# Performance work log

Hardware: AMD Instinct MI355X
Metric: run time of the kernel (lower is better)

## Reference

```python
import jax, jax.numpy as jnp
import numpy as np

N_NODES = 50000
N_EDGES = 600000
D_FEAT = 128


def setup_inputs() -> dict:
    key = jax.random.key(0)
    ks = jax.random.split(key, 10)
    x = jax.random.normal(ks[0], (N_NODES, D_FEAT), dtype=jnp.float32)
    src = jax.random.randint(ks[1], (N_EDGES,), 0, N_NODES, dtype=jnp.int32)
    dst = jax.random.randint(ks[2], (N_EDGES,), 0, N_NODES, dtype=jnp.int32)
    w1 = jax.random.normal(ks[3], (1, D_FEAT), dtype=jnp.float32) * 0.05
    Wd1 = jax.random.normal(ks[4], (D_FEAT, 64), dtype=jnp.float32) * 0.05
    b1 = jnp.zeros((64,), dtype=jnp.float32)
    w2 = jax.random.normal(ks[5], (1, 64), dtype=jnp.float32) * 0.05
    Wd2 = jax.random.normal(ks[6], (64, 32), dtype=jnp.float32) * 0.05
    b2 = jnp.zeros((32,), dtype=jnp.float32)
    Wout = jax.random.normal(ks[7], (32, 4), dtype=jnp.float32) * 0.05
    bout = jnp.zeros((4,), dtype=jnp.float32)
    return {"x": x, "src": src, "dst": dst, "w1": w1, "Wd1": Wd1, "b1": b1,
            "w2": w2, "Wd2": Wd2, "b2": b2, "Wout": Wout, "bout": bout}


def _spmm(src, dst, h):
    # A @ h for COO adjacency (edge src -> dst contributes h[src] into row dst)
    return jax.ops.segment_sum(h[src], dst, num_segments=N_NODES)


def reference(x, src, dst, w1, Wd1, b1, w2, Wd2, b2, Wout, bout):
    # input_layer is an Input wrapper: identity. Dropout is identity at inference.
    h = _spmm(src, dst, x) * w1          # GraphLayer 1: SpMM + elementwise scale
    h = h @ Wd1 + b1                     # Dense(64), linear activation
    h = _spmm(src, dst, h) * w2          # GraphLayer 2
    h = h @ Wd2 + b2                     # Dense(32)
    logits = h @ Wout + bout             # Dense(4)
    return jax.nn.softmax(logits, axis=-1)
```

## Files before the change

### kernel.cpp

```cpp
#include <hip/hip_runtime.h>
#include <hip/hip_bf16.h>

#define D_FEAT 128
#define NP 64
#define NP_SHIFT 6
#define P_PARTS 782
#define CAP 1024
#define EPB 2048


__global__ __launch_bounds__(256) void fused_xw_bucket_kernel(
    const float4* __restrict__ x4,
    const int* __restrict__ src,
    const int* __restrict__ dst,
    const float* __restrict__ w1,  const float* __restrict__ Wd1,
    const float* __restrict__ b1,  const float* __restrict__ w2,
    const float* __restrict__ Wd2, const float* __restrict__ b2,
    const float* __restrict__ Wout, const float* __restrict__ bout,
    int* __restrict__ partFill, int* __restrict__ edgeBuf,
    float* __restrict__ gc, float4* __restrict__ u4,
    int nN, int nE, int xwBlocks)
{
    __shared__ int sm[2 * P_PARTS];
    int t = threadIdx.x;

    if ((int)blockIdx.x < xwBlocks) {
        float* T2   = (float*)sm;
        float* Wall = (float*)sm + 256;
        {
            int m = t >> 2, j = t & 3;
            float s = 0.f;
            for (int p = 0; p < 32; ++p) s += Wd2[m * 32 + p] * Wout[p * 4 + j];
            T2[t] = w2[m] * s;
        }
        __syncthreads();
        for (int idx = t; idx < 512; idx += 256) {
            int k = idx >> 2, j = idx & 3;
            float s = 0.f;
            for (int m = 0; m < 64; ++m) s += Wd1[k * 64 + m] * T2[m * 4 + j];
            Wall[idx] = w1[k] * s;
        }
        if (blockIdx.x == 0 && t < 4) {
            float s = 0.f;
            for (int m = 0; m < 64; ++m) s += b1[m] * T2[m * 4 + t];
            gc[t] = s;
            float s2 = 0.f;
            for (int p = 0; p < 32; ++p) s2 += b2[p] * Wout[p * 4 + t];
            gc[4 + t] = s2 + bout[t];
        }
        __syncthreads();
        int r = blockIdx.x * 256 + t;
        if (r < nN) {
            const float4* W = (const float4*)Wall;
            float4 acc = make_float4(0.f, 0.f, 0.f, 0.f);
            #pragma unroll 8
            for (int k4 = 0; k4 < 32; ++k4) {
                float4 xv = x4[(size_t)r * 32 + k4];
                float4 w0 = W[4 * k4 + 0];
                float4 wv1 = W[4 * k4 + 1];
                float4 wv2 = W[4 * k4 + 2];
                float4 wv3 = W[4 * k4 + 3];
                acc.x += xv.x * w0.x + xv.y * wv1.x + xv.z * wv2.x + xv.w * wv3.x;
                acc.y += xv.x * w0.y + xv.y * wv1.y + xv.z * wv2.y + xv.w * wv3.y;
                acc.z += xv.x * w0.z + xv.y * wv1.z + xv.z * wv2.z + xv.w * wv3.z;
                acc.w += xv.x * w0.w + xv.y * wv1.w + xv.z * wv2.w + xv.w * wv3.w;
            }
            u4[r] = acc;
        }
    } else {
        int b = blockIdx.x - xwBlocks;
        int* hist = sm;
        int* base = sm + P_PARTS;
        for (int p = t; p < P_PARTS; p += 256) hist[p] = 0;
        __syncthreads();
        int beg = b * EPB + t;
        int end = min(b * EPB + EPB, nE);
        for (int i = beg; i < end; i += 256)
            atomicAdd(&hist[dst[i] >> NP_SHIFT], 1);
        __syncthreads();
        for (int p = t; p < P_PARTS; p += 256) {
            int h = hist[p];
            base[p] = h ? atomicAdd(&partFill[p], h) : 0;
        }
        __syncthreads();
        for (int i = beg; i < end; i += 256) {
            int d = dst[i];
            int p = d >> NP_SHIFT;
            int rank = atomicSub(&hist[p], 1) - 1;
            int pos = base[p] + rank;
            if (pos < CAP)
                edgeBuf[p * CAP + pos] = src[i] | ((d & (NP - 1)) << 16);
        }
    }
}

__global__ __launch_bounds__(256) void spmm_part_kernel(
    const int* __restrict__ partFill,
    const int* __restrict__ edgeBuf,
    const float4* __restrict__ in4,
    const float* __restrict__ gc, int gcOff,
    float4* __restrict__ out4, int nN, int doSoftmax)
{
    __shared__ float acc[NP * 4];
    int t = threadIdx.x, p = blockIdx.x;
    acc[t] = 0.f;
    __syncthreads();
    int n = min(partFill[p], CAP);
    const int* eb = edgeBuf + p * CAP;
    for (int i = t; i < n; i += 256) {
        int e = eb[i];
        float4 val = in4[e & 0xFFFF];
        int dl = e >> 16;
        atomicAdd(&acc[dl * 4 + 0], val.x);
        atomicAdd(&acc[dl * 4 + 1], val.y);
        atomicAdd(&acc[dl * 4 + 2], val.z);
        atomicAdd(&acc[dl * 4 + 3], val.w);
    }
    __syncthreads();
    if (t < NP) {
        int node = p * NP + t;
        if (node < nN) {
            float4 a = ((const float4*)acc)[t];
            float lx = a.x + gc[gcOff + 0];
            float ly = a.y + gc[gcOff + 1];
            float lz = a.z + gc[gcOff + 2];
            float lw = a.w + gc[gcOff + 3];
            if (doSoftmax) {
                float m = fmaxf(fmaxf(lx, ly), fmaxf(lz, lw));
                float ex = __expf(lx - m);
                float ey = __expf(ly - m);
                float ez = __expf(lz - m);
                float ew = __expf(lw - m);
                float r = 1.f / (ex + ey + ez + ew);
                out4[node] = make_float4(ex * r, ey * r, ez * r, ew * r);
            } else {
                out4[node] = make_float4(lx, ly, lz, lw);
            }
        }
    }
}

extern "C" void kernel_launch(void* const* d_in, const int* in_sizes, int n_in,
                              void* d_out, int out_size, void* d_ws, size_t ws_size,
                              hipStream_t stream)
{
    const float* x    = (const float*)d_in[0];
    const int*   src  = (const int*)d_in[1];
    const int*   dst  = (const int*)d_in[2];
    const float* w1   = (const float*)d_in[3];
    const float* Wd1  = (const float*)d_in[4];
    const float* b1   = (const float*)d_in[5];
    const float* w2   = (const float*)d_in[6];
    const float* Wd2  = (const float*)d_in[7];
    const float* b2   = (const float*)d_in[8];
    const float* Wout = (const float*)d_in[9];
    const float* bout = (const float*)d_in[10];

    const int nE = in_sizes[1];
    const int nN = in_sizes[0] / D_FEAT;

    float* ws = (float*)d_ws;
    float* gc = ws;
    float* u  = ws + 16;
    float* v  = u + (size_t)nN * 4;
    int* partFill = (int*)(v + (size_t)nN * 4);
    int* edgeBuf  = partFill + ((P_PARTS + 63) & ~63);

    const int xwBlocks = (nN + 255) / 256;
    const int bkBlocks = (nE + EPB - 1) / EPB;

    hipMemsetAsync(partFill, 0, P_PARTS * sizeof(int), stream);
    fused_xw_bucket_kernel<<<xwBlocks + bkBlocks, 256, 0, stream>>>(
        (const float4*)x, src, dst, w1, Wd1, b1, w2, Wd2, b2, Wout, bout,
        partFill, edgeBuf, gc, (float4*)u, nN, nE, xwBlocks);
    spmm_part_kernel<<<P_PARTS, 256, 0, stream>>>(partFill, edgeBuf,
                                                  (const float4*)u, gc, 0,
                                                  (float4*)v, nN, 0);
    spmm_part_kernel<<<P_PARTS, 256, 0, stream>>>(partFill, edgeBuf,
                                                  (const float4*)v, gc, 4,
                                                  (float4*)d_out, nN, 1);
}
```

Before: 143.9 us.

## Replace partition bucketing with direct global-atomic edge scatter and separate softmax

Drops the dst-partition bucketing pass and the per-partition shared-memory SpMM, and instead scatters each edge directly into the node outputs with global float atomics, processing two edges per thread. The dense projection now gives each node row to 32 lanes with coalesced loads and a shuffle reduction, and it pre-initialises the outputs with the folded bias constants so the atomics can accumulate on top. The softmax moves into its own small kernel. This removes the bucketing and the CAP truncation, which silently dropped edges when a partition held more than 1024, but it trades them for many contended global atomics on random addresses and one extra launch.

```diff
diff --git a/kernel.cpp b/kernel.cpp
--- a/kernel.cpp
+++ b/kernel.cpp
@@ -1,142 +1,124 @@
 #include <hip/hip_runtime.h>
-#include <hip/hip_bf16.h>
 
 #define D_FEAT 128
-#define NP 64
-#define NP_SHIFT 6
-#define P_PARTS 782
-#define CAP 1024
-#define EPB 2048
 
 
-__global__ __launch_bounds__(256) void fused_xw_bucket_kernel(
+__global__ __launch_bounds__(256) void fold_xw_init_kernel(
     const float4* __restrict__ x4,
-    const int* __restrict__ src,
-    const int* __restrict__ dst,
     const float* __restrict__ w1,  const float* __restrict__ Wd1,
     const float* __restrict__ b1,  const float* __restrict__ w2,
     const float* __restrict__ Wd2, const float* __restrict__ b2,
     const float* __restrict__ Wout, const float* __restrict__ bout,
-    int* __restrict__ partFill, int* __restrict__ edgeBuf,
-    float* __restrict__ gc, float4* __restrict__ u4,
-    int nN, int nE, int xwBlocks)
+    float4* __restrict__ u4, float4* __restrict__ v4, float4* __restrict__ l4,
+    int nN)
 {
-    __shared__ int sm[2 * P_PARTS];
+    __shared__ float  T2[256];
+    __shared__ float4 W4[128];
+    __shared__ float4 gcs[2];
     int t = threadIdx.x;
 
-    if ((int)blockIdx.x < xwBlocks) {
-        float* T2   = (float*)sm;
-        float* Wall = (float*)sm + 256;
-        {
-            int m = t >> 2, j = t & 3;
-            float s = 0.f;
-            for (int p = 0; p < 32; ++p) s += Wd2[m * 32 + p] * Wout[p * 4 + j];
-            T2[t] = w2[m] * s;
+    {
+        int m = t >> 2, j = t & 3;
+        float s = 0.f;
+        for (int p = 0; p < 32; ++p) s += Wd2[m * 32 + p] * Wout[p * 4 + j];
+        T2[t] = w2[m] * s;
+    }
+    __syncthreads();
+    for (int idx = t; idx < 512; idx += 256) {
+        int k = idx >> 2, j = idx & 3;
+        float s = 0.f;
+        for (int m = 0; m < 64; ++m) s += Wd1[k * 64 + m] * T2[m * 4 + j];
+        ((float*)W4)[idx] = w1[k] * s;
+    }
+    if (t < 4) {
+        float s = 0.f;
+        for (int m = 0; m < 64; ++m) s += b1[m] * T2[m * 4 + t];
+        ((float*)gcs)[t] = s;
+        float s2 = 0.f;
+        for (int p = 0; p < 32; ++p) s2 += b2[p] * Wout[p * 4 + t];
+        ((float*)gcs)[4 + t] = s2 + bout[t];
+    }
+    __syncthreads();
+
+    int lane = t & 63;
+    int k4 = lane & 31;
+    float4 wa = W4[4 * k4 + 0];
+    float4 wb = W4[4 * k4 + 1];
+    float4 wc = W4[4 * k4 + 2];
+    float4 wd = W4[4 * k4 + 3];
+    float4 gv = gcs[0], cv = gcs[1];
+
+    int R0 = blockIdx.x * 256;
+    #pragma unroll 4
+    for (int p = 0; p < 32; ++p) {
+        int fi = R0 * 32 + p * 256 + t;
+        int r  = R0 + p * 8 + (t >> 5);
+        bool ok = r < nN;
+        float4 xv = ok ? x4[fi] : make_float4(0.f, 0.f, 0.f, 0.f);
+        float4 a;
+        a.x = xv.x * wa.x + xv.y * wb.x + xv.z * wc.x + xv.w * wd.x;
+        a.y = xv.x * wa.y + xv.y * wb.y + xv.z * wc.y + xv.w * wd.y;
+        a.z = xv.x * wa.z + xv.y * wb.z + xv.z * wc.z + xv.w * wd.z;
+        a.w = xv.x * wa.w + xv.y * wb.w + xv.z * wc.w + xv.w * wd.w;
+        for (int m = 16; m >= 1; m >>= 1) {
+            a.x += __shfl_xor(a.x, m);
+            a.y += __shfl_xor(a.y, m);
+            a.z += __shfl_xor(a.z, m);
+            a.w += __shfl_xor(a.w, m);
         }
-        __syncthreads();
-        for (int idx = t; idx < 512; idx += 256) {
-            int k = idx >> 2, j = idx & 3;
-            float s = 0.f;
-            for (int m = 0; m < 64; ++m) s += Wd1[k * 64 + m] * T2[m * 4 + j];
-            Wall[idx] = w1[k] * s;
-        }
-        if (blockIdx.x == 0 && t < 4) {
-            float s = 0.f;
-            for (int m = 0; m < 64; ++m) s += b1[m] * T2[m * 4 + t];
-            gc[t] = s;
-            float s2 = 0.f;
-            for (int p = 0; p < 32; ++p) s2 += b2[p] * Wout[p * 4 + t];
-            gc[4 + t] = s2 + bout[t];
-        }
-        __syncthreads();
-        int r = blockIdx.x * 256 + t;
-        if (r < nN) {
-            const float4* W = (const float4*)Wall;
-            float4 acc = make_float4(0.f, 0.f, 0.f, 0.f);
-            #pragma unroll 8
-            for (int k4 = 0; k4 < 32; ++k4) {
-                float4 xv = x4[(size_t)r * 32 + k4];
-                float4 w0 = W[4 * k4 + 0];
-                float4 wv1 = W[4 * k4 + 1];
-                float4 wv2 = W[4 * k4 + 2];
-                float4 wv3 = W[4 * k4 + 3];
-                acc.x += xv.x * w0.x + xv.y * wv1.x + xv.z * wv2.x + xv.w * wv3.x;
-                acc.y += xv.x * w0.y + xv.y * wv1.y + xv.z * wv2.y + xv.w * wv3.y;
-                acc.z += xv.x * w0.z + xv.y * wv1.z + xv.z * wv2.z + xv.w * wv3.z;
-                acc.w += xv.x * w0.w + xv.y * wv1.w + xv.z * wv2.w + xv.w * wv3.w;
-            }
-            u4[r] = acc;
-        }
-    } else {
-        int b = blockIdx.x - xwBlocks;
-        int* hist = sm;
-        int* base = sm + P_PARTS;
-        for (int p = t; p < P_PARTS; p += 256) hist[p] = 0;
-        __syncthreads();
-        int beg = b * EPB + t;
-        int end = min(b * EPB + EPB, nE);
-        for (int i = beg; i < end; i += 256)
-            atomicAdd(&hist[dst[i] >> NP_SHIFT], 1);
-        __syncthreads();
-        for (int p = t; p < P_PARTS; p += 256) {
-            int h = hist[p];
-            base[p] = h ? atomicAdd(&partFill[p], h) : 0;
-        }
-        __syncthreads();
-        for (int i = beg; i < end; i += 256) {
-            int d = dst[i];
-            int p = d >> NP_SHIFT;
-            int rank = atomicSub(&hist[p], 1) - 1;
-            int pos = base[p] + rank;
-            if (pos < CAP)
-                edgeBuf[p * CAP + pos] = src[i] | ((d & (NP - 1)) << 16);
+        if (ok && (lane & 31) == 0) {
+            u4[r] = a;
+            v4[r] = gv;
+            l4[r] = cv;
         }
     }
 }
 
-__global__ __launch_bounds__(256) void spmm_part_kernel(
-    const int* __restrict__ partFill,
-    const int* __restrict__ edgeBuf,
-    const float4* __restrict__ in4,
-    const float* __restrict__ gc, int gcOff,
-    float4* __restrict__ out4, int nN, int doSoftmax)
+__global__ __launch_bounds__(256) void edge_kernel(
+    const int2* __restrict__ src2, const int2* __restrict__ dst2,
+    const float4* __restrict__ in4, float* __restrict__ outp,
+    int nPair, int nE)
 {
-    __shared__ float acc[NP * 4];
-    int t = threadIdx.x, p = blockIdx.x;
-    acc[t] = 0.f;
-    __syncthreads();
-    int n = min(partFill[p], CAP);
-    const int* eb = edgeBuf + p * CAP;
-    for (int i = t; i < n; i += 256) {
-        int e = eb[i];
-        float4 val = in4[e & 0xFFFF];
-        int dl = e >> 16;
-        atomicAdd(&acc[dl * 4 + 0], val.x);
-        atomicAdd(&acc[dl * 4 + 1], val.y);
-        atomicAdd(&acc[dl * 4 + 2], val.z);
-        atomicAdd(&acc[dl * 4 + 3], val.w);
+    int i = blockIdx.x * 256 + threadIdx.x;
+    if (i < nPair) {
+        int2 s = src2[i];
+        int2 d = dst2[i];
+        float4 a = in4[s.x];
+        float4 b = in4[s.y];
+        atomicAdd(&outp[4 * d.x + 0], a.x);
+        atomicAdd(&outp[4 * d.x + 1], a.y);
+        atomicAdd(&outp[4 * d.x + 2], a.z);
+        atomicAdd(&outp[4 * d.x + 3], a.w);
+        atomicAdd(&outp[4 * d.y + 0], b.x);
+        atomicAdd(&outp[4 * d.y + 1], b.y);
+        atomicAdd(&outp[4 * d.y + 2], b.z);
+        atomicAdd(&outp[4 * d.y + 3], b.w);
     }
-    __syncthreads();
-    if (t < NP) {
-        int node = p * NP + t;
-        if (node < nN) {
-            float4 a = ((const float4*)acc)[t];
-            float lx = a.x + gc[gcOff + 0];
-            float ly = a.y + gc[gcOff + 1];
-            float lz = a.z + gc[gcOff + 2];
-            float lw = a.w + gc[gcOff + 3];
-            if (doSoftmax) {
-                float m = fmaxf(fmaxf(lx, ly), fmaxf(lz, lw));
-                float ex = __expf(lx - m);
-                float ey = __expf(ly - m);
-                float ez = __expf(lz - m);
-                float ew = __expf(lw - m);
-                float r = 1.f / (ex + ey + ez + ew);
-                out4[node] = make_float4(ex * r, ey * r, ez * r, ew * r);
-            } else {
-                out4[node] = make_float4(lx, ly, lz, lw);
-            }
-        }
+    if (i == 0 && (nE & 1)) {
+        int e = nE - 1;
+        int s = ((const int*)src2)[e];
+        int d = ((const int*)dst2)[e];
+        float4 a = in4[s];
+        atomicAdd(&outp[4 * d + 0], a.x);
+        atomicAdd(&outp[4 * d + 1], a.y);
+        atomicAdd(&outp[4 * d + 2], a.z);
+        atomicAdd(&outp[4 * d + 3], a.w);
+    }
+}
+
+__global__ __launch_bounds__(256) void softmax_kernel(
+    const float4* __restrict__ l4, float4* __restrict__ out4, int nN)
+{
+    int i = blockIdx.x * 256 + threadIdx.x;
+    if (i < nN) {
+        float4 l = l4[i];
+        float m  = fmaxf(fmaxf(l.x, l.y), fmaxf(l.z, l.w));
+        float ex = __expf(l.x - m);
+        float ey = __expf(l.y - m);
+        float ez = __expf(l.z - m);
+        float ew = __expf(l.w - m);
+        float r  = 1.f / (ex + ey + ez + ew);
+        out4[i] = make_float4(ex * r, ey * r, ez * r, ew * r);
     }
 }
 
@@ -160,23 +142,21 @@
     const int nN = in_sizes[0] / D_FEAT;
 
     float* ws = (float*)d_ws;
-    float* gc = ws;
-    float* u  = ws + 16;
+    float* u  = ws;
     float* v  = u + (size_t)nN * 4;
-    int* partFill = (int*)(v + (size_t)nN * 4);
-    int* edgeBuf  = partFill + ((P_PARTS + 63) & ~63);
+    float* l  = v + (size_t)nN * 4;
 
-    const int xwBlocks = (nN + 255) / 256;
-    const int bkBlocks = (nE + EPB - 1) / EPB;
+    const int nodeBlocks = (nN + 255) / 256;
+    const int nPair      = nE >> 1;
+    const int edgeBlocks = (nPair + 255) / 256;
 
-    hipMemsetAsync(partFill, 0, P_PARTS * sizeof(int), stream);
-    fused_xw_bucket_kernel<<<xwBlocks + bkBlocks, 256, 0, stream>>>(
-        (const float4*)x, src, dst, w1, Wd1, b1, w2, Wd2, b2, Wout, bout,
-        partFill, edgeBuf, gc, (float4*)u, nN, nE, xwBlocks);
-    spmm_part_kernel<<<P_PARTS, 256, 0, stream>>>(partFill, edgeBuf,
-                                                  (const float4*)u, gc, 0,
-                                                  (float4*)v, nN, 0);
-    spmm_part_kernel<<<P_PARTS, 256, 0, stream>>>(partFill, edgeBuf,
-                                                  (const float4*)v, gc, 4,
-                                                  (float4*)d_out, nN, 1);
+    fold_xw_init_kernel<<<nodeBlocks, 256, 0, stream>>>(
+        (const float4*)x, w1, Wd1, b1, w2, Wd2, b2, Wout, bout,
+        (float4*)u, (float4*)v, (float4*)l, nN);
+    edge_kernel<<<edgeBlocks, 256, 0, stream>>>(
+        (const int2*)src, (const int2*)dst, (const float4*)u, v, nPair, nE);
+    edge_kernel<<<edgeBlocks, 256, 0, stream>>>(
+        (const int2*)src, (const int2*)dst, (const float4*)v, l, nPair, nE);
+    softmax_kernel<<<nodeBlocks, 256, 0, stream>>>(
+        (const float4*)l, (float4*)d_out, nN);
 }
```

Result: slower. 361.0 us (+150.9%).

## Vectorize edge loads, pad partition counters, and transpose shared accumulators

Applied to the files above, without the earlier changes.

The bucketing phase now loads eight dst and src indices per thread with int4 vector loads held in registers. Previously each edge was read from global memory twice, once for the histogram and once for the scatter. Global partition fill counters are padded to 64-byte stride, which is meant to cut contention between atomics on the same cache line. The SpMM shared accumulator is transposed to [4][72], which is meant to reduce LDS bank conflicts on the atomic adds. The trade-offs are a larger memset and workspace offset and somewhat higher register use.

```diff
diff --git a/kernel.cpp b/kernel.cpp
--- a/kernel.cpp
+++ b/kernel.cpp
@@ -1,5 +1,4 @@
 #include <hip/hip_runtime.h>
-#include <hip/hip_bf16.h>
 
 #define D_FEAT 128
 #define NP 64
@@ -7,6 +6,7 @@
 #define P_PARTS 782
 #define CAP 1024
 #define EPB 2048
+#define PF_STRIDE 16
 
 
 __global__ __launch_bounds__(256) void fused_xw_bucket_kernel(
@@ -21,7 +21,7 @@
     float* __restrict__ gc, float4* __restrict__ u4,
     int nN, int nE, int xwBlocks)
 {
-    __shared__ int sm[2 * P_PARTS];
+    __shared__ __align__(16) int sm[2 * P_PARTS];
     int t = threadIdx.x;
 
     if ((int)blockIdx.x < xwBlocks) {
@@ -56,7 +56,7 @@
             #pragma unroll 8
             for (int k4 = 0; k4 < 32; ++k4) {
                 float4 xv = x4[(size_t)r * 32 + k4];
-                float4 w0 = W[4 * k4 + 0];
+                float4 w0  = W[4 * k4 + 0];
                 float4 wv1 = W[4 * k4 + 1];
                 float4 wv2 = W[4 * k4 + 2];
                 float4 wv3 = W[4 * k4 + 3];
@@ -73,23 +73,42 @@
         int* base = sm + P_PARTS;
         for (int p = t; p < P_PARTS; p += 256) hist[p] = 0;
         __syncthreads();
-        int beg = b * EPB + t;
-        int end = min(b * EPB + EPB, nE);
-        for (int i = beg; i < end; i += 256)
-            atomicAdd(&hist[dst[i] >> NP_SHIFT], 1);
+
+        int beg = b * EPB;
+        int i0  = beg + 8 * t;
+        int4 d0 = make_int4(0,0,0,0), d1 = make_int4(0,0,0,0);
+        int4 s0 = make_int4(0,0,0,0), s1 = make_int4(0,0,0,0);
+        if (i0 + 3 < nE) { d0 = ((const int4*)dst)[(beg >> 2) + 2 * t];
+                           s0 = ((const int4*)src)[(beg >> 2) + 2 * t]; }
+        else for (int j = 0; i0 + j < nE && j < 4; ++j) {
+            ((int*)&d0)[j] = dst[i0 + j]; ((int*)&s0)[j] = src[i0 + j];
+        }
+        if (i0 + 7 < nE) { d1 = ((const int4*)dst)[(beg >> 2) + 2 * t + 1];
+                           s1 = ((const int4*)src)[(beg >> 2) + 2 * t + 1]; }
+        else for (int j = 4; i0 + j < nE && j < 8; ++j) {
+            ((int*)&d1)[j - 4] = dst[i0 + j]; ((int*)&s1)[j - 4] = src[i0 + j];
+        }
+        int dd[8] = {d0.x, d0.y, d0.z, d0.w, d1.x, d1.y, d1.z, d1.w};
+        int ss[8] = {s0.x, s0.y, s0.z, s0.w, s1.x, s1.y, s1.z, s1.w};
+
+        #pragma unroll
+        for (int j = 0; j < 8; ++j)
+            if (i0 + j < nE) atomicAdd(&hist[dd[j] >> NP_SHIFT], 1);
         __syncthreads();
         for (int p = t; p < P_PARTS; p += 256) {
             int h = hist[p];
-            base[p] = h ? atomicAdd(&partFill[p], h) : 0;
-        }
-        __syncthreads();
-        for (int i = beg; i < end; i += 256) {
-            int d = dst[i];
-            int p = d >> NP_SHIFT;
-            int rank = atomicSub(&hist[p], 1) - 1;
-            int pos = base[p] + rank;
-            if (pos < CAP)
-                edgeBuf[p * CAP + pos] = src[i] | ((d & (NP - 1)) << 16);
+            base[p] = h ? atomicAdd(&partFill[p * PF_STRIDE], h) : 0;
+        }
+        __syncthreads();
+        #pragma unroll
+        for (int j = 0; j < 8; ++j) {
+            if (i0 + j < nE) {
+                int d = dd[j], pp = d >> NP_SHIFT;
+                int rank = atomicSub(&hist[pp], 1) - 1;
+                int pos = base[pp] + rank;
+                if (pos < CAP)
+                    edgeBuf[pp * CAP + pos] = ss[j] | ((d & (NP - 1)) << 16);
+            }
         }
     }
 }
@@ -101,30 +120,29 @@
     const float* __restrict__ gc, int gcOff,
     float4* __restrict__ out4, int nN, int doSoftmax)
 {
-    __shared__ float acc[NP * 4];
+    __shared__ float acc[4][72];
     int t = threadIdx.x, p = blockIdx.x;
-    acc[t] = 0.f;
+    for (int i = t; i < 288; i += 256) ((float*)acc)[i] = 0.f;
     __syncthreads();
-    int n = min(partFill[p], CAP);
+    int n = min(partFill[p * PF_STRIDE], CAP);
     const int* eb = edgeBuf + p * CAP;
     for (int i = t; i < n; i += 256) {
         int e = eb[i];
         float4 val = in4[e & 0xFFFF];
         int dl = e >> 16;
-        atomicAdd(&acc[dl * 4 + 0], val.x);
-        atomicAdd(&acc[dl * 4 + 1], val.y);
-        atomicAdd(&acc[dl * 4 + 2], val.z);
-        atomicAdd(&acc[dl * 4 + 3], val.w);
+        atomicAdd(&acc[0][dl], val.x);
+        atomicAdd(&acc[1][dl], val.y);
+        atomicAdd(&acc[2][dl], val.z);
+        atomicAdd(&acc[3][dl], val.w);
     }
     __syncthreads();
     if (t < NP) {
         int node = p * NP + t;
         if (node < nN) {
-            float4 a = ((const float4*)acc)[t];
-            float lx = a.x + gc[gcOff + 0];
-            float ly = a.y + gc[gcOff + 1];
-            float lz = a.z + gc[gcOff + 2];
-            float lw = a.w + gc[gcOff + 3];
+            float lx = acc[0][t] + gc[gcOff + 0];
+            float ly = acc[1][t] + gc[gcOff + 1];
+            float lz = acc[2][t] + gc[gcOff + 2];
+            float lw = acc[3][t] + gc[gcOff + 3];
             if (doSoftmax) {
                 float m = fmaxf(fmaxf(lx, ly), fmaxf(lz, lw));
                 float ex = __expf(lx - m);
@@ -164,12 +182,12 @@
     float* u  = ws + 16;
     float* v  = u + (size_t)nN * 4;
     int* partFill = (int*)(v + (size_t)nN * 4);
-    int* edgeBuf  = partFill + ((P_PARTS + 63) & ~63);
+    int* edgeBuf  = partFill + P_PARTS * PF_STRIDE;
 
     const int xwBlocks = (nN + 255) / 256;
     const int bkBlocks = (nE + EPB - 1) / EPB;
 
-    hipMemsetAsync(partFill, 0, P_PARTS * sizeof(int), stream);
+    hipMemsetAsync(partFill, 0, P_PARTS * PF_STRIDE * sizeof(int), stream);
     fused_xw_bucket_kernel<<<xwBlocks + bkBlocks, 256, 0, stream>>>(
         (const float4*)x, src, dst, w1, Wd1, b1, w2, Wd2, b2, Wout, bout,
         partFill, edgeBuf, gc, (float4*)u, nN, nE, xwBlocks);
```

After: 145.3 us. About the same (+1.0%).
